# Optimization experiments

Hardware: AMD Instinct MI355X
Metric: run time of the kernel (lower is better)

## Reference

```python
import math
import jax, jax.numpy as jnp
import numpy as np

B, T, C = 4, 2048, 1024
N_HEAD = 16
HEAD_DIM = C // N_HEAD


def setup_inputs() -> dict:
    key = jax.random.key(0)
    k1, k2, k3 = jax.random.split(key, 3)
    x = jax.random.normal(k1, (B, T, C), dtype=jnp.float32)
    # nn.Linear weights: (out_features, in_features); init scale ~1/sqrt(C)
    w_attn = jax.random.normal(k2, (3 * C, C), dtype=jnp.float32) / math.sqrt(C)
    w_proj = jax.random.normal(k3, (C, C), dtype=jnp.float32) / math.sqrt(C)
    return {"x": x, "w_attn": w_attn, "w_proj": w_proj}


def reference(x, w_attn, w_proj):
    Bx, Tx, Cx = x.shape
    qkv = x @ w_attn.T  # (B,T,3C)
    q, k, v = jnp.split(qkv, 3, axis=2)
    # (B,T,H,D) -> (B,H,T,D)
    q = q.reshape(Bx, Tx, N_HEAD, HEAD_DIM).transpose(0, 2, 1, 3)
    k = k.reshape(Bx, Tx, N_HEAD, HEAD_DIM).transpose(0, 2, 1, 3)
    v = v.reshape(Bx, Tx, N_HEAD, HEAD_DIM).transpose(0, 2, 1, 3)
    scale = 1.0 / math.sqrt(HEAD_DIM)
    att = jnp.einsum("bhqd,bhkd->bhqk", q, k) * scale
    causal = jnp.tril(jnp.ones((Tx, Tx), dtype=bool))
    att = jnp.where(causal[None, None, :, :], att, -jnp.inf)
    att = jax.nn.softmax(att, axis=-1)
    out = jnp.einsum("bhqk,bhkd->bhqd", att, v)
    out = out.transpose(0, 2, 1, 3).reshape(Bx, Tx, Cx)
    return out @ w_proj.T
```

## Files before the change

kernel.cpp:

```cpp
#include <hip/hip_runtime.h>
#include <hip/hip_bf16.h>


typedef __attribute__((ext_vector_type(8))) short bf16x8;
typedef __attribute__((ext_vector_type(4))) float f32x4;
typedef unsigned short ushort_t;

#if __has_builtin(__builtin_amdgcn_exp2f)
#define EXP2(x) __builtin_amdgcn_exp2f(x)
#else
#define EXP2(x) exp2f(x)
#endif

__device__ inline ushort_t f2bf(float f) {
    union { float f; unsigned int u; } x; x.f = f;
    return (ushort_t)((x.u + 0x7fffu + ((x.u >> 16) & 1u)) >> 16);
}

__device__ inline ushort_t f2bf_fast(float f) {
    union { float f; unsigned int u; } x; x.f = f;
    return (ushort_t)((x.u + 0x8000u) >> 16);
}

__device__ inline bf16x8 load8_f32_to_bf16(const float* p) {
    float4 f0 = *(const float4*)p;
    float4 f1 = *(const float4*)(p + 4);
    bf16x8 r;
    r[0] = (short)f2bf(f0.x); r[1] = (short)f2bf(f0.y);
    r[2] = (short)f2bf(f0.z); r[3] = (short)f2bf(f0.w);
    r[4] = (short)f2bf(f1.x); r[5] = (short)f2bf(f1.y);
    r[6] = (short)f2bf(f1.z); r[7] = (short)f2bf(f1.w);
    return r;
}

__device__ inline void gl2lds16(const ushort_t* g, ushort_t* l) {
    __builtin_amdgcn_global_load_lds(
        (const __attribute__((address_space(1))) unsigned int*)g,
        (__attribute__((address_space(3))) unsigned int*)l,
        16, 0, 0);
}

__global__ void cvt3(const float* __restrict__ a, long n8a,
                     const float* __restrict__ b, long n8b,
                     const float* __restrict__ c, long n8c,
                     ushort_t* __restrict__ out) {
    long i = (long)blockIdx.x * 256 + threadIdx.x;
    const float* src; long off;
    if (i < n8a) { src = a; off = i; }
    else if (i < n8a + n8b) { src = b; off = i - n8a; }
    else if (i < n8a + n8b + n8c) { src = c; off = i - n8a - n8b; }
    else return;
    *(bf16x8*)(out + i * 8) = load8_f32_to_bf16(src + off * 8);
}

__global__ void fill_zero_f32(float* out, int n) {
    int i = blockIdx.x * 256 + threadIdx.x;
    if (i < n) out[i] = 0.0f;
}

#define QK_LOG2E_SCALE 0.18033688011112042f

#define QBK 64
#define ABUF (128 * 64)
#define BBUF (256 * 64)
#define TBUF (ABUF + BBUF)

template <int EPI>
__global__ __launch_bounds__(512) void gemm_sw(
        const ushort_t* __restrict__ A, const ushort_t* __restrict__ B,
        void* __restrict__ Cp, void* __restrict__ Cp2,
        int M, int N, int K) {
    __shared__ ushort_t S[3 * TBUF];

    const int tid  = threadIdx.x;
    const int lane = tid & 63;
    const int w    = tid >> 6;
    const int quad = lane >> 4;
    const int l16  = lane & 15;
    const int wr   = w >> 2;
    const int wc   = w & 3;

    const int nbx = N >> 8;
    const int cpx = gridDim.x >> 3;
    const int swz = ((int)blockIdx.x & 7) * cpx + ((int)blockIdx.x >> 3);
    const int bm = (swz / nbx) << 7;
    const int bn = (swz % nbx) << 8;

    const int nt = K >> 6;

    const int srow = lane >> 3;
    const int soct = (lane & 7) ^ srow;
    const ushort_t* Ag = A + (size_t)(bm + w * 16 + srow) * K + soct * 8;
    const ushort_t* Bg = B + (size_t)(bn + w * 32 + srow) * K + soct * 8;

    auto stage = [&](int kt, ushort_t* d) {
        const size_t ko = (size_t)kt * QBK;
        gl2lds16(Ag + ko,                  d + w * 1024);
        gl2lds16(Ag + ko + (size_t)8 * K,  d + w * 1024 + 512);
#pragma unroll
        for (int j = 0; j < 4; j++)
            gl2lds16(Bg + ko + (size_t)(j * 8) * K,
                     d + ABUF + w * 2048 + j * 512);
    };

    const int sl7 = l16 & 7;
    const int ca0 = ((quad)     ^ sl7) * 8;
    const int ca1 = ((quad + 4) ^ sl7) * 8;
    const int arow = (wr * 64 + l16) * 64;
    const int brow = ABUF + (wc * 64 + l16) * 64;

    f32x4 acc[4][4] = {};

    stage(0, S);
    stage(1, S + TBUF);
    __asm__ __volatile__("s_waitcnt vmcnt(6)" ::: "memory");
    __builtin_amdgcn_s_barrier();

    int bc = 0, bs = 2;
    for (int kt = 0; kt < nt; kt++) {
        if (kt + 2 < nt) stage(kt + 2, S + bs * TBUF);

        const ushort_t* Sb = S + bc * TBUF;
        bf16x8 af[4][2], bfr[4][2];
#pragma unroll
        for (int mi = 0; mi < 4; mi++) {
            af[mi][0] = *(const bf16x8*)(Sb + arow + mi * 1024 + ca0);
            af[mi][1] = *(const bf16x8*)(Sb + arow + mi * 1024 + ca1);
        }
#pragma unroll
        for (int ni = 0; ni < 4; ni++) {
            bfr[ni][0] = *(const bf16x8*)(Sb + brow + ni * 1024 + ca0);
            bfr[ni][1] = *(const bf16x8*)(Sb + brow + ni * 1024 + ca1);
        }

        __builtin_amdgcn_s_setprio(1);
#pragma unroll
        for (int mi = 0; mi < 4; mi++)
#pragma unroll
            for (int ni = 0; ni < 4; ni++)
#pragma unroll
                for (int kk = 0; kk < 2; kk++)
                    acc[mi][ni] = __builtin_amdgcn_mfma_f32_16x16x32_bf16(
                        af[mi][kk], bfr[ni][kk], acc[mi][ni], 0, 0, 0);
        __builtin_amdgcn_s_setprio(0);

        if (kt + 2 < nt)
            __asm__ __volatile__("s_waitcnt vmcnt(6)" ::: "memory");
        else if (kt + 1 < nt)
            __asm__ __volatile__("s_waitcnt vmcnt(0)" ::: "memory");
        __builtin_amdgcn_s_barrier();

        bc = (bc + 1 == 3) ? 0 : bc + 1;
        bs = (bs + 1 == 3) ? 0 : bs + 1;
    }

    const int colbase = bn + wc * 64;
    const int rowbase = bm + wr * 64 + quad * 4;
    if constexpr (EPI == 1) {
#pragma unroll
        for (int mi = 0; mi < 4; mi++) {
            const int row = rowbase + mi * 16;
            float* cr = (float*)Cp + (size_t)row * N + colbase + l16;
#pragma unroll
            for (int r = 0; r < 4; r++)
#pragma unroll
                for (int ni = 0; ni < 4; ni++)
                    cr[(size_t)r * N + ni * 16] = acc[mi][ni][r];
        }
    } else {
        if (colbase < 2048) {
            const float qs = (colbase < 1024) ? QK_LOG2E_SCALE : 1.0f;
#pragma unroll
            for (int mi = 0; mi < 4; mi++) {
                const int row = rowbase + mi * 16;
                ushort_t* qp = (ushort_t*)Cp + (size_t)row * 2048 + colbase + l16;
#pragma unroll
                for (int r = 0; r < 4; r++)
#pragma unroll
                    for (int ni = 0; ni < 4; ni++)
                        qp[(size_t)r * 2048 + ni * 16] = f2bf(acc[mi][ni][r] * qs);
            }
        } else {
#pragma unroll
            for (int mi = 0; mi < 4; mi++) {
                const int row = rowbase + mi * 16;
                const int bb = row >> 11, tt = row & 2047;
#pragma unroll
                for (int ni = 0; ni < 4; ni++) {
                    const int vc = colbase + ni * 16 + l16 - 2048;
                    const int hh = vc >> 6, dd = vc & 63;
                    ushort_t* vp = (ushort_t*)Cp2 +
                        ((((size_t)bb * 16 + hh) * 64 + dd) * 2048) + tt;
#pragma unroll
                    for (int r = 0; r < 4; r++)
                        vp[r] = f2bf(acc[mi][ni][r]);
                }
            }
        }
    }
}

#define BM 128
#define BN 128
#define BK 64
#define LDK 72

template <bool A_F32, bool B_F32, int EPI>
__global__ __launch_bounds__(256) void gemm_nt(
        const void* __restrict__ Ap, const void* __restrict__ Bp,
        void* __restrict__ Cp, void* __restrict__ Cp2,
        int M, int N, int K) {
    __shared__ ushort_t As[BM * LDK];
    __shared__ ushort_t Bs[BN * LDK];

    const int tid  = threadIdx.x;
    const int lane = tid & 63;
    const int w    = tid >> 6;
    const int quad = lane >> 4;
    const int l16  = lane & 15;

    const int bm = blockIdx.y * BM;
    const int bn = blockIdx.x * BN;
    const int wm = (w & 1) * 64;
    const int wn = (w >> 1) * 64;

    f32x4 acc[4][4] = {};

    const int lrow = tid >> 3;
    const int lcol = (tid & 7) * 8;

    bf16x8 pa[4], pb[4];
#pragma unroll
    for (int i = 0; i < 4; i++) {
        const int ra = lrow + i * 32;
        if constexpr (A_F32)
            pa[i] = load8_f32_to_bf16((const float*)Ap + (size_t)(bm + ra) * K + lcol);
        else
            pa[i] = *(const bf16x8*)((const ushort_t*)Ap + (size_t)(bm + ra) * K + lcol);
        if constexpr (B_F32)
            pb[i] = load8_f32_to_bf16((const float*)Bp + (size_t)(bn + ra) * K + lcol);
        else
            pb[i] = *(const bf16x8*)((const ushort_t*)Bp + (size_t)(bn + ra) * K + lcol);
    }

    for (int k0 = 0; k0 < K; k0 += BK) {
        __syncthreads();
#pragma unroll
        for (int i = 0; i < 4; i++) {
            *(bf16x8*)&As[(lrow + i * 32) * LDK + lcol] = pa[i];
            *(bf16x8*)&Bs[(lrow + i * 32) * LDK + lcol] = pb[i];
        }
        __syncthreads();

        if (k0 + BK < K) {
            const int kn = k0 + BK + lcol;
#pragma unroll
            for (int i = 0; i < 4; i++) {
                const int ra = lrow + i * 32;
                if constexpr (A_F32)
                    pa[i] = load8_f32_to_bf16((const float*)Ap + (size_t)(bm + ra) * K + kn);
                else
                    pa[i] = *(const bf16x8*)((const ushort_t*)Ap + (size_t)(bm + ra) * K + kn);
                if constexpr (B_F32)
                    pb[i] = load8_f32_to_bf16((const float*)Bp + (size_t)(bn + ra) * K + kn);
                else
                    pb[i] = *(const bf16x8*)((const ushort_t*)Bp + (size_t)(bn + ra) * K + kn);
            }
        }

#pragma unroll
        for (int ks = 0; ks < BK; ks += 32) {
            bf16x8 af[4], bfr[4];
#pragma unroll
            for (int i = 0; i < 4; i++)
                af[i] = *(const bf16x8*)&As[(wm + i * 16 + l16) * LDK + ks + quad * 8];
#pragma unroll
            for (int i = 0; i < 4; i++)
                bfr[i] = *(const bf16x8*)&Bs[(wn + i * 16 + l16) * LDK + ks + quad * 8];
#pragma unroll
            for (int mi = 0; mi < 4; mi++)
#pragma unroll
                for (int ni = 0; ni < 4; ni++)
                    acc[mi][ni] = __builtin_amdgcn_mfma_f32_16x16x32_bf16(
                        af[mi], bfr[ni], acc[mi][ni], 0, 0, 0);
        }
    }

#pragma unroll
    for (int mi = 0; mi < 4; mi++) {
        const int row0 = bm + wm + mi * 16 + quad * 4;
#pragma unroll
        for (int r = 0; r < 4; r++) {
            const int row = row0 + r;
            if constexpr (EPI == 1) {
                float* crow = (float*)Cp + (size_t)row * N + bn + wn;
#pragma unroll
                for (int ni = 0; ni < 4; ni++)
                    crow[ni * 16 + l16] = acc[mi][ni][r];
            } else {
                if (bn < 2048) {
                    const float qs = (bn < 1024) ? QK_LOG2E_SCALE : 1.0f;
                    ushort_t* crow = (ushort_t*)Cp + (size_t)row * 2048 + bn + wn;
#pragma unroll
                    for (int ni = 0; ni < 4; ni++)
                        crow[ni * 16 + l16] = f2bf(acc[mi][ni][r] * qs);
                } else {
                    ushort_t* vt = (ushort_t*)Cp2;
                    const int bb = row >> 11, tt = row & 2047;
#pragma unroll
                    for (int ni = 0; ni < 4; ni++) {
                        const int vc = bn + wn + ni * 16 + l16 - 2048;
                        const int hh = vc >> 6, dd = vc & 63;
                        vt[(((size_t)bb * 16 + hh) * 64 + dd) * 2048 + tt] =
                            f2bf(acc[mi][ni][r]);
                    }
                }
            }
        }
    }
}

#define AT_T 2048
#define PLD 72

__global__ __launch_bounds__(256) void attn4(
        const ushort_t* __restrict__ qk,
        const ushort_t* __restrict__ vt,
        ushort_t* __restrict__ attout) {
    const int bh   = blockIdx.x;
    const int qblk = (gridDim.y - 1) - blockIdx.y;
    const int b    = bh >> 4;
    const int h    = bh & 15;

    const int tid  = threadIdx.x;
    const int lane = tid & 63;
    const int w    = tid >> 6;
    const int quad = lane >> 4;
    const int l16  = lane & 15;
    const int sw   = l16 & 7;

    __shared__ ushort_t Ks[64 * 64];
    __shared__ ushort_t Vs[80 * 64];
    __shared__ ushort_t Ps[4][32 * PLD];

    for (int i = tid; i < 16 * 64; i += 256) Vs[64 * 64 + i] = 0;
    if (tid < 64) Vs[64 * 64 + tid] = 0x3F80;

    const ushort_t* qp = qk + (size_t)b * AT_T * 2048 + h * 64;
    const ushort_t* kp = qp + 1024;
    const ushort_t* vp = vt + (size_t)bh * 64 * 2048;

    const int Q0 = qblk * 128 + w * 16;

    bf16x8 aq[2][2];
#pragma unroll
    for (int s = 0; s < 2; s++) {
        const ushort_t* qrow = qp + (size_t)(Q0 + s * 64 + l16) * 2048;
        aq[s][0] = *(const bf16x8*)(qrow + quad * 8);
        aq[s][1] = *(const bf16x8*)(qrow + 32 + quad * 8);
    }

    f32x4 o[2][5] = {};

    const int lr8 = lane >> 3;
    const int cbg = ((lane & 7) ^ lr8) * 8;

    const int nk = 2 * qblk + 2;
    for (int kt = 0; kt < nk; kt++) {
        const int k0 = kt * 64;
        if (kt) __syncthreads();
#pragma unroll
        for (int j = 0; j < 2; j++) {
            gl2lds16(kp + (size_t)(k0 + w * 16 + j * 8 + lr8) * 2048 + cbg,
                     &Ks[(w * 16 + j * 8) * 64]);
            gl2lds16(vp + (size_t)(w * 16 + j * 8 + lr8) * 2048 + k0 + cbg,
                     &Vs[(w * 16 + j * 8) * 64]);
        }
        __syncthreads();

        f32x4 s0[4], s1[4];
#pragma unroll
        for (int c = 0; c < 4; c++) {
            s0[c][0] = -8.0f; s0[c][1] = -8.0f; s0[c][2] = -8.0f; s0[c][3] = -8.0f;
            s1[c] = s0[c];
#pragma unroll
            for (int ks = 0; ks < 2; ks++) {
                const int cs = ((quad + 4 * ks) ^ sw) * 8;
                bf16x8 bk = *(const bf16x8*)&Ks[(c * 16 + l16) * 64 + cs];
                s0[c] = __builtin_amdgcn_mfma_f32_16x16x32_bf16(aq[0][ks], bk, s0[c], 0, 0, 0);
                s1[c] = __builtin_amdgcn_mfma_f32_16x16x32_bf16(aq[1][ks], bk, s1[c], 0, 0, 0);
            }
        }

        if (kt >= 2 * qblk) {
            const int q0r = Q0 + quad * 4;
#pragma unroll
            for (int c = 0; c < 4; c++) {
                const int kcol = k0 + c * 16 + l16;
#pragma unroll
                for (int r = 0; r < 4; r++)
                    if (kcol > q0r + r) s0[c][r] = -__builtin_inff();
            }
        }
        if (kt == 2 * qblk + 1) {
            const int q1r = Q0 + 64 + quad * 4;
#pragma unroll
            for (int c = 0; c < 4; c++) {
                const int kcol = k0 + c * 16 + l16;
#pragma unroll
                for (int r = 0; r < 4; r++)
                    if (kcol > q1r + r) s1[c][r] = -__builtin_inff();
            }
        }

#pragma unroll
        for (int c = 0; c < 4; c++)
#pragma unroll
            for (int r = 0; r < 4; r++) {
                Ps[w][(quad * 4 + r) * PLD + c * 16 + l16] = f2bf_fast(EXP2(s0[c][r]));
                Ps[w][(16 + quad * 4 + r) * PLD + c * 16 + l16] = f2bf_fast(EXP2(s1[c][r]));
            }

        __asm__ __volatile__("s_waitcnt lgkmcnt(0)" ::: "memory");

#pragma unroll
        for (int ks = 0; ks < 2; ks++) {
            const int cs = ((quad + 4 * ks) ^ sw) * 8;
            bf16x8 ap0 = *(const bf16x8*)&Ps[w][l16 * PLD + ks * 32 + quad * 8];
            bf16x8 ap1 = *(const bf16x8*)&Ps[w][(16 + l16) * PLD + ks * 32 + quad * 8];
#pragma unroll
            for (int n = 0; n < 5; n++) {
                bf16x8 bv = *(const bf16x8*)&Vs[(n * 16 + l16) * 64 + cs];
                o[0][n] = __builtin_amdgcn_mfma_f32_16x16x32_bf16(ap0, bv, o[0][n], 0, 0, 0);
                o[1][n] = __builtin_amdgcn_mfma_f32_16x16x32_bf16(ap1, bv, o[1][n], 0, 0, 0);
            }
        }
    }

#pragma unroll
    for (int s = 0; s < 2; s++) {
        ushort_t* op = attout + (size_t)(b * AT_T + Q0 + s * 64 + quad * 4) * 1024 + h * 64;
#pragma unroll
        for (int r = 0; r < 4; r++) {
            const float l = __shfl(o[s][4][r], lane & 48, 64);
            const float inv = 1.0f / fmaxf(l, 1e-30f);
            ushort_t* orow = op + (size_t)r * 1024;
#pragma unroll
            for (int n = 0; n < 4; n++)
                orow[n * 16 + l16] = f2bf(o[s][n][r] * inv);
        }
    }
}

extern "C" void kernel_launch(void* const* d_in, const int* in_sizes, int n_in,
                              void* d_out, int out_size, void* d_ws, size_t ws_size,
                              hipStream_t stream) {
    const float* x      = (const float*)d_in[0];
    const float* w_attn = (const float*)d_in[1];
    const float* w_proj = (const float*)d_in[2];
    float* out = (float*)d_out;

    const int M = 8192, C = 1024;
    const size_t E_QK  = (size_t)M * 2048;
    const size_t E_VT  = (size_t)4 * 16 * 64 * 2048;
    const size_t E_ATT = (size_t)M * 1024;
    const size_t E_X   = (size_t)M * 1024;
    const size_t E_WA  = (size_t)3072 * 1024;
    const size_t E_WP  = (size_t)1024 * 1024;
    const size_t need_mid  = (E_QK + E_VT + E_ATT) * 2;
    const size_t need_full = need_mid + (E_X + E_WA + E_WP) * 2;

    if (ws_size < need_mid) {
        fill_zero_f32<<<(out_size + 255) / 256, 256, 0, stream>>>(out, out_size);
        return;
    }

    ushort_t* qk  = (ushort_t*)d_ws;
    ushort_t* vt  = qk + E_QK;
    ushort_t* att = vt + E_VT;

    if (ws_size >= need_full) {
        ushort_t* xb  = att + E_ATT;
        const long n8x = (long)(E_X / 8), n8a = (long)(E_WA / 8), n8p = (long)(E_WP / 8);
        const long n8  = n8x + n8a + n8p;
        cvt3<<<(int)((n8 + 255) / 256), 256, 0, stream>>>(
            x, n8x, w_attn, n8a, w_proj, n8p, xb);

        ushort_t* wab = xb + E_X;
        ushort_t* wpb = wab + E_WA;
        gemm_sw<2><<<dim3((M / 128) * (3 * C / 256)), 512, 0, stream>>>(
            xb, wab, qk, vt, M, 3 * C, C);
        attn4<<<dim3(64, 16), 256, 0, stream>>>(qk, vt, att);
        gemm_sw<1><<<dim3((M / 128) * (C / 256)), 512, 0, stream>>>(
            att, wpb, out, nullptr, M, C, C);
    } else {
        gemm_nt<true, true, 2><<<dim3(3 * C / BN, M / BM), 256, 0, stream>>>(
            x, w_attn, qk, vt, M, 3 * C, C);
        attn4<<<dim3(64, 16), 256, 0, stream>>>(qk, vt, att);
        gemm_nt<false, true, 1><<<dim3(C / BN, M / BM), 256, 0, stream>>>(
            att, w_proj, out, nullptr, M, C, C);
    }
}
```

Baseline: 235.9 us.

## Split GEMM k-tile into two halves interleaving LDS reads, prefetch and MFMA

The GEMM main loop now processes each k-tile in two half-steps. Each half loads its A/B fragments from LDS and issues part of the global-to-LDS prefetch for tile kt+2, then runs 16 MFMAs. The aim is to interleave memory issue with compute and lower fragment register pressure, ping-pong style. It adds extra barriers per iteration, which may add synchronisation stalls.

```diff
diff --git a/kernel.cpp b/kernel.cpp
--- a/kernel.cpp
+++ b/kernel.cpp
@@ -118,30 +118,55 @@
 
     int bc = 0, bs = 2;
     for (int kt = 0; kt < nt; kt++) {
-        if (kt + 2 < nt) stage(kt + 2, S + bs * TBUF);
-
         const ushort_t* Sb = S + bc * TBUF;
-        bf16x8 af[4][2], bfr[4][2];
-#pragma unroll
-        for (int mi = 0; mi < 4; mi++) {
-            af[mi][0] = *(const bf16x8*)(Sb + arow + mi * 1024 + ca0);
-            af[mi][1] = *(const bf16x8*)(Sb + arow + mi * 1024 + ca1);
-        }
-#pragma unroll
-        for (int ni = 0; ni < 4; ni++) {
-            bfr[ni][0] = *(const bf16x8*)(Sb + brow + ni * 1024 + ca0);
-            bfr[ni][1] = *(const bf16x8*)(Sb + brow + ni * 1024 + ca1);
-        }
-
+        ushort_t* sd = S + bs * TBUF;
+        const bool pf = (kt + 2 < nt);
+        const size_t ko = (size_t)(kt + 2) * QBK;
+
+        bf16x8 af[4], bfr[4];
+
+#pragma unroll
+        for (int mi = 0; mi < 4; mi++)
+            af[mi]  = *(const bf16x8*)(Sb + arow + mi * 1024 + ca0);
+#pragma unroll
+        for (int ni = 0; ni < 4; ni++)
+            bfr[ni] = *(const bf16x8*)(Sb + brow + ni * 1024 + ca0);
+        if (pf) {
+            gl2lds16(Ag + ko,                 sd + w * 1024);
+            gl2lds16(Ag + ko + (size_t)8 * K, sd + w * 1024 + 512);
+            gl2lds16(Bg + ko,                 sd + ABUF + w * 2048);
+        }
+        __builtin_amdgcn_s_barrier();
         __builtin_amdgcn_s_setprio(1);
 #pragma unroll
         for (int mi = 0; mi < 4; mi++)
 #pragma unroll
             for (int ni = 0; ni < 4; ni++)
-#pragma unroll
-                for (int kk = 0; kk < 2; kk++)
-                    acc[mi][ni] = __builtin_amdgcn_mfma_f32_16x16x32_bf16(
-                        af[mi][kk], bfr[ni][kk], acc[mi][ni], 0, 0, 0);
+                acc[mi][ni] = __builtin_amdgcn_mfma_f32_16x16x32_bf16(
+                    af[mi], bfr[ni], acc[mi][ni], 0, 0, 0);
+        __builtin_amdgcn_s_setprio(0);
+        __builtin_amdgcn_s_barrier();
+
+#pragma unroll
+        for (int mi = 0; mi < 4; mi++)
+            af[mi]  = *(const bf16x8*)(Sb + arow + mi * 1024 + ca1);
+#pragma unroll
+        for (int ni = 0; ni < 4; ni++)
+            bfr[ni] = *(const bf16x8*)(Sb + brow + ni * 1024 + ca1);
+        if (pf) {
+#pragma unroll
+            for (int j = 1; j < 4; j++)
+                gl2lds16(Bg + ko + (size_t)(j * 8) * K,
+                         sd + ABUF + w * 2048 + j * 512);
+        }
+        __builtin_amdgcn_s_barrier();
+        __builtin_amdgcn_s_setprio(1);
+#pragma unroll
+        for (int mi = 0; mi < 4; mi++)
+#pragma unroll
+            for (int ni = 0; ni < 4; ni++)
+                acc[mi][ni] = __builtin_amdgcn_mfma_f32_16x16x32_bf16(
+                    af[mi], bfr[ni], acc[mi][ni], 0, 0, 0);
         __builtin_amdgcn_s_setprio(0);
 
         if (kt + 2 < nt)
```

Measured after the change: 245.9 us. 4.2% more time.

## Replace 128x256 triple-buffered GEMM with 128x128 double-buffered 4-wave tile

Applied to the files above, without the earlier changes.

Both projection GEMMs move from a 512-thread kernel with a 128x256 tile and three LDS stages to a 256-thread kernel with a 128x128 tile and two LDS stages. Each of the four waves still computes a 64x64 sub-tile. The aim is more, smaller blocks and lower LDS use per block, which should raise occupancy and spread work better across CUs. The cost is less operand reuse per block and a shallower prefetch pipeline, since the loop now waits with vmcnt(0) every iteration.

```diff
diff --git a/kernel.cpp b/kernel.cpp
--- a/kernel.cpp
+++ b/kernel.cpp
@@ -60,67 +60,62 @@
 
 #define QK_LOG2E_SCALE 0.18033688011112042f
 
-#define QBK 64
-#define ABUF (128 * 64)
-#define BBUF (256 * 64)
-#define TBUF (ABUF + BBUF)
+#define OVBUF 16384
 
 template <int EPI>
-__global__ __launch_bounds__(512) void gemm_sw(
+__global__ __launch_bounds__(256) void gemm_ov(
         const ushort_t* __restrict__ A, const ushort_t* __restrict__ B,
         void* __restrict__ Cp, void* __restrict__ Cp2,
         int M, int N, int K) {
-    __shared__ ushort_t S[3 * TBUF];
+    __shared__ ushort_t S[2 * OVBUF];
 
     const int tid  = threadIdx.x;
     const int lane = tid & 63;
     const int w    = tid >> 6;
     const int quad = lane >> 4;
     const int l16  = lane & 15;
-    const int wr   = w >> 2;
-    const int wc   = w & 3;
-
-    const int nbx = N >> 8;
+    const int wm   = (w & 1) * 64;
+    const int wn   = (w >> 1) * 64;
+
+    const int nbx = N >> 7;
     const int cpx = gridDim.x >> 3;
     const int swz = ((int)blockIdx.x & 7) * cpx + ((int)blockIdx.x >> 3);
     const int bm = (swz / nbx) << 7;
-    const int bn = (swz % nbx) << 8;
+    const int bn = (swz % nbx) << 7;
 
     const int nt = K >> 6;
 
     const int srow = lane >> 3;
     const int soct = (lane & 7) ^ srow;
-    const ushort_t* Ag = A + (size_t)(bm + w * 16 + srow) * K + soct * 8;
+    const ushort_t* Ag = A + (size_t)(bm + w * 32 + srow) * K + soct * 8;
     const ushort_t* Bg = B + (size_t)(bn + w * 32 + srow) * K + soct * 8;
 
-    auto stage = [&](int kt, ushort_t* d) {
-        const size_t ko = (size_t)kt * QBK;
-        gl2lds16(Ag + ko,                  d + w * 1024);
-        gl2lds16(Ag + ko + (size_t)8 * K,  d + w * 1024 + 512);
-#pragma unroll
-        for (int j = 0; j < 4; j++)
-            gl2lds16(Bg + ko + (size_t)(j * 8) * K,
-                     d + ABUF + w * 2048 + j * 512);
+    auto stage = [&](int kt) {
+        ushort_t* d = S + (kt & 1) * OVBUF;
+        const size_t ko = (size_t)kt * 64;
+#pragma unroll
+        for (int j = 0; j < 4; j++) {
+            gl2lds16(Ag + ko + (size_t)(j * 8) * K, d + w * 2048 + j * 512);
+            gl2lds16(Bg + ko + (size_t)(j * 8) * K, d + 8192 + w * 2048 + j * 512);
+        }
     };
 
     const int sl7 = l16 & 7;
     const int ca0 = ((quad)     ^ sl7) * 8;
     const int ca1 = ((quad + 4) ^ sl7) * 8;
-    const int arow = (wr * 64 + l16) * 64;
-    const int brow = ABUF + (wc * 64 + l16) * 64;
+    const int arow = (wm + l16) * 64;
+    const int brow = 8192 + (wn + l16) * 64;
 
     f32x4 acc[4][4] = {};
 
-    stage(0, S);
-    stage(1, S + TBUF);
-    __asm__ __volatile__("s_waitcnt vmcnt(6)" ::: "memory");
+    stage(0);
+    __asm__ __volatile__("s_waitcnt vmcnt(0)" ::: "memory");
     __builtin_amdgcn_s_barrier();
 
-    int bc = 0, bs = 2;
     for (int kt = 0; kt < nt; kt++) {
-        if (kt + 2 < nt) stage(kt + 2, S + bs * TBUF);
-
-        const ushort_t* Sb = S + bc * TBUF;
+        if (kt + 1 < nt) stage(kt + 1);
+
+        const ushort_t* Sb = S + (kt & 1) * OVBUF;
         bf16x8 af[4][2], bfr[4][2];
 #pragma unroll
         for (int mi = 0; mi < 4; mi++) {
@@ -144,18 +139,12 @@
                         af[mi][kk], bfr[ni][kk], acc[mi][ni], 0, 0, 0);
         __builtin_amdgcn_s_setprio(0);
 
-        if (kt + 2 < nt)
-            __asm__ __volatile__("s_waitcnt vmcnt(6)" ::: "memory");
-        else if (kt + 1 < nt)
-            __asm__ __volatile__("s_waitcnt vmcnt(0)" ::: "memory");
+        __asm__ __volatile__("s_waitcnt vmcnt(0)" ::: "memory");
         __builtin_amdgcn_s_barrier();
-
-        bc = (bc + 1 == 3) ? 0 : bc + 1;
-        bs = (bs + 1 == 3) ? 0 : bs + 1;
-    }
-
-    const int colbase = bn + wc * 64;
-    const int rowbase = bm + wr * 64 + quad * 4;
+    }
+
+    const int colbase = bn + wn;
+    const int rowbase = bm + wm + quad * 4;
     if constexpr (EPI == 1) {
 #pragma unroll
         for (int mi = 0; mi < 4; mi++) {
@@ -488,10 +477,10 @@
 
         ushort_t* wab = xb + E_X;
         ushort_t* wpb = wab + E_WA;
-        gemm_sw<2><<<dim3((M / 128) * (3 * C / 256)), 512, 0, stream>>>(
+        gemm_ov<2><<<dim3((M / 128) * (3 * C / 128)), 256, 0, stream>>>(
             xb, wab, qk, vt, M, 3 * C, C);
         attn4<<<dim3(64, 16), 256, 0, stream>>>(qk, vt, att);
-        gemm_sw<1><<<dim3((M / 128) * (C / 256)), 512, 0, stream>>>(
+        gemm_ov<1><<<dim3((M / 128) * (C / 128)), 256, 0, stream>>>(
             att, wpb, out, nullptr, M, C, C);
     } else {
         gemm_nt<true, true, 2><<<dim3(3 * C / BN, M / BM), 256, 0, stream>>>(
```

Measured after the change: 232.5 us. About the same (-1.4%).
